# Performance work log

Measured on AMD Instinct MI355X. Metric: run time of the kernel, lower is better.

## Reference

```python
import jax, jax.numpy as jnp
import numpy as np

B, T, D, G, E, V = 32, 1024, 512, 256, 8, 8192


def setup_inputs() -> dict:
    key = jax.random.key(0)
    k1, k2, k3, k4, k5 = jax.random.split(key, 5)
    return {
        "gate_features": jax.random.normal(k1, (B, G), dtype=jnp.float32),
        "input_features": jax.random.normal(k2, (B, T, D), dtype=jnp.float32),
        "Wg": jax.random.normal(k3, (G, E), dtype=jnp.float32) * 0.02,
        "bg": jnp.zeros((E,), dtype=jnp.float32),
        "We": jax.random.normal(k4, (E, D, V), dtype=jnp.float32) * 0.02,
        "be": jnp.zeros((E, V), dtype=jnp.float32),
        "target_ids": jax.random.randint(k5, (B, T), 0, V, dtype=jnp.int64),
    }


def reference(gate_features, input_features, Wg, bg, We, be, target_ids):
    # ---- Router: linear gate -> softmax probs -> top-1 assignment ----
    router_logits = gate_features @ Wg + bg            # [B, E]
    probs = jax.nn.softmax(router_logits, axis=-1)     # [B, E]
    assignments = jnp.argmax(router_logits, axis=-1)   # [B]

    # ---- Dispatch: gather each sample's expert parameters ----
    W_sel = We[assignments]                            # [B, D, V]
    b_sel = be[assignments]                            # [B, V]

    # ---- Expert compute: linear LM head + cross-entropy loss ----
    logits = jnp.einsum("btd,bdv->btv", input_features, W_sel) + b_sel[:, None, :]
    logp = jax.nn.log_softmax(logits, axis=-1)         # [B, T, V]
    nll = -jnp.take_along_axis(logp, target_ids[..., None], axis=-1)[..., 0]  # [B, T]
    ce_per_sample = nll.mean(axis=-1)                  # [B]

    # ---- Combine: total_loss = sum over experts of per-expert mean loss ----
    sums = jax.ops.segment_sum(ce_per_sample, assignments, num_segments=E)   # [E]
    counts = jax.ops.segment_sum(jnp.ones_like(ce_per_sample), assignments, num_segments=E)
    loss_per_expert = jnp.where(counts > 0, sums / jnp.maximum(counts, 1.0), 0.0)
    total_loss = loss_per_expert.sum()

    return total_loss, assignments, probs
```

## Files before the change

kernel.cpp:

```cpp
#include <hip/hip_runtime.h>

#define NB 32
#define NT 1024
#define ND 512
#define NG 256
#define NE 8
#define NV 8192
#define NROW (NB * NT)

#define XBF_BYTES   (33554432)
#define WT_BYTES    (67108864)
#define PSUM_BYTES  (8388608)
#define TL_BYTES    (131072)

#define BM2 256
#define BN2 256
#define NCT (NV / BN2)

typedef float f32x4 __attribute__((ext_vector_type(4)));
typedef __bf16 bf16x8 __attribute__((ext_vector_type(8)));
typedef unsigned short ushort8_v __attribute__((ext_vector_type(8)));
typedef unsigned int u32_g __attribute__((address_space(1)));
typedef unsigned int u32_l __attribute__((address_space(3)));
typedef unsigned short ushort_t;

__device__ __forceinline__ void g2l16(void* lds, const void* g) {
    __builtin_amdgcn_global_load_lds((const u32_g*)g, (u32_l*)lds, 16, 0, 0);
}

__device__ __forceinline__ unsigned short f2bf(float f) {
    unsigned int u = __float_as_uint(f);
    unsigned int r = (u + 0x7fffu + ((u >> 16) & 1u)) >> 16;
    return (unsigned short)r;
}

__global__ void k_convx(const float4* __restrict__ in, ushort_t* __restrict__ out4, int n4,
                        const float* __restrict__ gate, const float* __restrict__ Wg,
                        const float* __restrict__ bg, float* __restrict__ out,
                        int* __restrict__ assign, int* __restrict__ counts) {
    int tid = threadIdx.x;
    if (blockIdx.x == 0) {
        __shared__ float lg[NB][NE];
        __shared__ int lam[NB];
        int b = tid >> 3, e = tid & 7;
        float acc = bg[e];
        const float* gr = gate + b * NG;
        for (int g = 0; g < NG; ++g) acc = fmaf(gr[g], Wg[g * NE + e], acc);
        lg[b][e] = acc;
        __syncthreads();
        if (tid < NB) {
            float mx = lg[tid][0]; int am = 0;
            for (int j = 1; j < NE; ++j) { float v = lg[tid][j]; if (v > mx) { mx = v; am = j; } }
            float den = 0.f, ex[NE];
            for (int j = 0; j < NE; ++j) { ex[j] = __expf(lg[tid][j] - mx); den += ex[j]; }
            float inv = 1.f / den;
            for (int j = 0; j < NE; ++j) out[1 + NB + tid * NE + j] = ex[j] * inv;
            out[1 + tid] = (float)am;
            assign[tid] = am;
            lam[tid] = am;
        }
        __syncthreads();
        if (tid == 0) {
            int c[NE] = {0,0,0,0,0,0,0,0};
            for (int i = 0; i < NB; ++i) c[lam[i]]++;
            for (int j = 0; j < NE; ++j) counts[j] = c[j];
            out[0] = 0.f;
        }
    }
    int i = blockIdx.x * blockDim.x + tid;
    int stride = gridDim.x * blockDim.x;
    for (; i < n4; i += stride) {
        float4 v = in[i];
        ushort4 o;
        o.x = f2bf(v.x); o.y = f2bf(v.y); o.z = f2bf(v.z); o.w = f2bf(v.w);
        ((ushort4*)out4)[i] = o;
    }
}

__global__ void k_transw(const float* __restrict__ We, ushort_t* __restrict__ Wt) {
    __shared__ float tile[64][68];
    int e = blockIdx.z, d0 = blockIdx.y * 64, v0 = blockIdx.x * 64;
    int tid = threadIdx.x;
    const float* src = We + (size_t)e * ND * NV + (size_t)d0 * NV + v0;
    int dr = tid >> 4;
    int c4 = tid & 15;
#pragma unroll
    for (int j = 0; j < 4; ++j) {
        int d = dr + 16 * j;
        float4 v = *(const float4*)(src + (size_t)d * NV + c4 * 4);
        *(float4*)&tile[d][((c4 ^ (d >> 3)) & 15) * 4] = v;
    }
    __syncthreads();
    ushort_t* dst = Wt + (size_t)e * NV * ND + (size_t)v0 * ND + d0;
    int vr = tid >> 3;
    int t8 = tid & 7;
#pragma unroll
    for (int j = 0; j < 2; ++j) {
        int v = vr + 32 * j;
        ushort8_v o;
#pragma unroll
        for (int i = 0; i < 8; ++i)
            o[i] = f2bf(tile[t8 * 8 + i][(((v >> 2) ^ t8) & 15) * 4 + (v & 3)]);
        *(ushort8_v*)(dst + (size_t)v * ND + t8 * 8) = o;
    }
}


#define BAR_MID() do { \
    asm volatile("" ::: "memory"); \
    __builtin_amdgcn_s_barrier(); \
    asm volatile("s_waitcnt lgkmcnt(0)" ::: "memory"); \
    __builtin_amdgcn_sched_barrier(0); } while (0)

#define BAR_END() do { \
    asm volatile("" ::: "memory"); \
    __builtin_amdgcn_s_barrier(); \
    asm volatile("" ::: "memory"); } while (0)

#define MFMA_QUAD(MH, NH) do { \
    __builtin_amdgcn_s_setprio(1); \
    _Pragma("unroll") \
    for (int m_ = 0; m_ < 4; ++m_) \
      _Pragma("unroll") \
      for (int n_ = 0; n_ < 2; ++n_) \
        _Pragma("unroll") \
        for (int ks_ = 0; ks_ < 2; ++ks_) \
          acc[(MH) * 4 + m_][(NH) * 2 + n_] = __builtin_amdgcn_mfma_f32_16x16x32_bf16( \
              af[m_][ks_], bfr[(NH) * 2 + n_][ks_], acc[(MH) * 4 + m_][(NH) * 2 + n_], 0, 0, 0); \
    __builtin_amdgcn_s_setprio(0); } while (0)

__global__ __launch_bounds__(512, 2)
void k_gemm(const ushort_t* __restrict__ Xbf, const ushort_t* __restrict__ Wtbf,
            const float* __restrict__ be, const int* __restrict__ assign,
            const int* __restrict__ tgt, float* __restrict__ psum,
            float* __restrict__ tl) {
    __shared__ alignas(16) char smem[136192];
    float* lws = (float*)(smem + 131072);
    int*   lt  = (int*)(smem + 135168);

    const int tid  = threadIdx.x;
    const int wid  = tid >> 6, lane = tid & 63;
    const int q = lane >> 4, ln = lane & 15;
    const int wr = wid >> 2, wc = wid & 3;

    const int bid = blockIdx.x;
    const int wg  = ((bid & 7) << 9) | (bid >> 3);
    const int ct  = wg >> 7;
    const int rt  = wg & 127;
    const int e   = assign[rt >> 2];
    const size_t eV = (size_t)e * NV;

    const int rquo = tid >> 3;
    const int scol = ((tid & 7) ^ (rquo & 7)) << 3;
    const ushort_t* gA = Xbf + (size_t)(rt * BM2 + rquo) * ND + scol;
    const ushort_t* gB = Wtbf + (eV + ct * BN2 + rquo) * ND + scol;
    char* ldsW = smem + wid * 1024;
    const int axor = ln & 7;

    if (tid < 256) lt[tid] = tgt[rt * BM2 + tid];

    f32x4 acc[8][4];
#pragma unroll
    for (int i = 0; i < 8; ++i)
#pragma unroll
        for (int j = 0; j < 4; ++j) acc[i][j] = (f32x4){0.f, 0.f, 0.f, 0.f};

#define STA(KT, BP, H) do { \
    char* d_ = ldsW + (BP) * 65536 + (H) * 16384; \
    const ushort_t* g_ = gA + (size_t)(H) * 128 * ND + (KT) * 64; \
    g2l16(d_, g_); g2l16(d_ + 8192, g_ + (size_t)64 * ND); } while (0)

#define STB(KT, BP, H) do { \
    char* d_ = ldsW + (BP) * 65536 + 32768 + (H) * 16384; \
    const ushort_t* g_ = gB + (size_t)(H) * 128 * ND + (KT) * 64; \
    g2l16(d_, g_); g2l16(d_ + 8192, g_ + (size_t)64 * ND); } while (0)

#define RDA(BP, MF, KS) \
    (*(const bf16x8*)(smem + (BP) * 65536 + wr * 16384 + \
                      ((MF) * 16 + ln) * 128 + ((((KS) * 4 + q) ^ axor) << 4)))

#define RDB(BP, NF, KS) \
    (*(const bf16x8*)(smem + (BP) * 65536 + 32768 + (wc >> 1) * 16384 + \
                      (((wc & 1) * 64 + (NF) * 16 + ln) * 128) + ((((KS) * 4 + q) ^ axor) << 4)))

    STB(0, 0, 0); STB(0, 0, 1); STA(0, 0, 0); STA(0, 0, 1);
    STB(1, 1, 0); STB(1, 1, 1);
    asm volatile("s_waitcnt vmcnt(4)" ::: "memory");
    __builtin_amdgcn_s_barrier();
    asm volatile("" ::: "memory");

    bf16x8 af[4][2];
    bf16x8 bfr[4][2];

#pragma unroll
    for (int kt = 0; kt < 8; ++kt) {
        const int p = kt & 1, np = p ^ 1;

#pragma unroll
        for (int m = 0; m < 4; ++m) { af[m][0] = RDA(p, m, 0); af[m][1] = RDA(p, m, 1); }
#pragma unroll
        for (int n = 0; n < 2; ++n) { bfr[n][0] = RDB(p, n, 0); bfr[n][1] = RDB(p, n, 1); }
        if (kt < 7) STA(kt + 1, np, 0);
        BAR_MID();
        MFMA_QUAD(0, 0);
        BAR_END();

#pragma unroll
        for (int n = 0; n < 2; ++n) { bfr[2 + n][0] = RDB(p, 2 + n, 0); bfr[2 + n][1] = RDB(p, 2 + n, 1); }
        if (kt < 7) STA(kt + 1, np, 1);
        BAR_MID();
        MFMA_QUAD(0, 1);
        BAR_END();

#pragma unroll
        for (int m = 0; m < 4; ++m) { af[m][0] = RDA(p, 4 + m, 0); af[m][1] = RDA(p, 4 + m, 1); }
        if (kt < 6) STB(kt + 2, p, 0);
        BAR_MID();
        MFMA_QUAD(1, 1);
        BAR_END();

        if (kt < 6) STB(kt + 2, p, 1);
        BAR_MID();
        MFMA_QUAD(1, 0);
        if (kt < 6)       { asm volatile("s_waitcnt vmcnt(4)" ::: "memory"); }
        else if (kt == 6) { asm volatile("s_waitcnt vmcnt(0)" ::: "memory"); }
        BAR_END();
    }

    const float LOG2E = 1.44269504088896f;
    int tcv[8][4];
#pragma unroll
    for (int mf = 0; mf < 8; ++mf)
#pragma unroll
        for (int r = 0; r < 4; ++r)
            tcv[mf][r] = lt[wr * 128 + mf * 16 + q * 4 + r];

    float partial[32];
#pragma unroll
    for (int i = 0; i < 32; ++i) partial[i] = 0.f;
#pragma unroll
    for (int nf = 0; nf < 4; ++nf) {
        int col = (ct << 8) + (wc << 6) + nf * 16 + ln;
        float br = be[eV + col];
        float eb = br * LOG2E;
#pragma unroll
        for (int mf = 0; mf < 8; ++mf)
#pragma unroll
            for (int r = 0; r < 4; ++r) {
                partial[mf * 4 + r] += exp2f(fmaf(acc[mf][nf][r], LOG2E, eb));
                if (col == tcv[mf][r])
                    tl[rt * BM2 + wr * 128 + mf * 16 + q * 4 + r] = acc[mf][nf][r] + br;
            }
    }
#pragma unroll
    for (int i = 0; i < 32; ++i) {
        float pv = partial[i];
        pv += __shfl_xor(pv, 1); pv += __shfl_xor(pv, 2);
        pv += __shfl_xor(pv, 4); pv += __shfl_xor(pv, 8);
        partial[i] = pv;
    }
    if (ln == 0) {
#pragma unroll
        for (int mf = 0; mf < 8; ++mf)
#pragma unroll
            for (int r = 0; r < 4; ++r)
                lws[wid * 128 + mf * 16 + q * 4 + r] = partial[mf * 4 + r];
    }
    __syncthreads();
    if (tid < 256) {
        int wrh = tid >> 7, idx = tid & 127;
        float s = lws[(wrh * 4 + 0) * 128 + idx] + lws[(wrh * 4 + 1) * 128 + idx]
                + lws[(wrh * 4 + 2) * 128 + idx] + lws[(wrh * 4 + 3) * 128 + idx];
        psum[(size_t)ct * NROW + rt * 256 + tid] = s;
    }
#undef STA
#undef STB
#undef RDA
#undef RDB
}

__global__ void k_loss(const float* __restrict__ psum, const float* __restrict__ tl,
                       const int* __restrict__ assign, const int* __restrict__ counts,
                       float* __restrict__ out) {
    int b = blockIdx.x, tid = threadIdx.x;
    float acc = 0.f;
#pragma unroll
    for (int j = 0; j < 4; ++j) {
        int t = j * 256 + tid;
        float s = 0.f;
        for (int ct = 0; ct < NCT; ++ct) s += psum[(size_t)ct * NROW + b * NT + t];
        acc += __logf(s) - tl[b * NT + t];
    }
    __shared__ float red[4];
    for (int off = 32; off; off >>= 1) acc += __shfl_down(acc, off);
    if ((tid & 63) == 0) red[tid >> 6] = acc;
    __syncthreads();
    if (tid == 0) {
        float nb = red[0] + red[1] + red[2] + red[3];
        float ce = nb * (1.0f / (float)NT);
        atomicAdd(out, ce / (float)counts[assign[b]]);
    }
}

extern "C" void kernel_launch(void* const* d_in, const int* in_sizes, int n_in,
                              void* d_out, int out_size, void* d_ws, size_t ws_size,
                              hipStream_t stream) {
    const float* gate = (const float*)d_in[0];
    const float* X    = (const float*)d_in[1];
    const float* Wg   = (const float*)d_in[2];
    const float* bg   = (const float*)d_in[3];
    const float* We   = (const float*)d_in[4];
    const float* be   = (const float*)d_in[5];
    const int*   tgt  = (const int*)d_in[6];
    float* out = (float*)d_out;

    char* ws = (char*)d_ws;
    ushort_t* Xbf  = (ushort_t*)ws;
    ushort_t* Wtbf = (ushort_t*)(ws + XBF_BYTES);
    float*    psum = (float*)(ws + XBF_BYTES + WT_BYTES);
    float*    tl   = (float*)(ws + XBF_BYTES + WT_BYTES + PSUM_BYTES);
    int*      assign = (int*)(ws + XBF_BYTES + WT_BYTES + PSUM_BYTES + TL_BYTES);
    int*      counts = assign + 32;

    k_convx<<<4096, 256, 0, stream>>>((const float4*)X, Xbf, NB * NT * ND / 4,
                                      gate, Wg, bg, out, assign, counts);
    k_transw<<<dim3(NV / 64, ND / 64, NE), 256, 0, stream>>>(We, Wtbf);
    k_gemm<<<(NROW / BM2) * (NV / BN2), 512, 0, stream>>>(Xbf, Wtbf, be, assign, tgt, psum, tl);
    k_loss<<<NB, 256, 0, stream>>>(psum, tl, assign, counts, out);
}
```

Baseline: 608.4 us.

## Merge weight transpose and input conversion into one prep kernel, stage bias/targets via LDS

```diff
diff --git a/kernel.cpp b/kernel.cpp
--- a/kernel.cpp
+++ b/kernel.cpp
@@ -34,74 +34,77 @@
     return (unsigned short)r;
 }
 
-__global__ void k_convx(const float4* __restrict__ in, ushort_t* __restrict__ out4, int n4,
-                        const float* __restrict__ gate, const float* __restrict__ Wg,
-                        const float* __restrict__ bg, float* __restrict__ out,
-                        int* __restrict__ assign, int* __restrict__ counts) {
-    int tid = threadIdx.x;
-    if (blockIdx.x == 0) {
-        __shared__ float lg[NB][NE];
-        __shared__ int lam[NB];
-        int b = tid >> 3, e = tid & 7;
-        float acc = bg[e];
-        const float* gr = gate + b * NG;
-        for (int g = 0; g < NG; ++g) acc = fmaf(gr[g], Wg[g * NE + e], acc);
-        lg[b][e] = acc;
-        __syncthreads();
-        if (tid < NB) {
-            float mx = lg[tid][0]; int am = 0;
-            for (int j = 1; j < NE; ++j) { float v = lg[tid][j]; if (v > mx) { mx = v; am = j; } }
-            float den = 0.f, ex[NE];
-            for (int j = 0; j < NE; ++j) { ex[j] = __expf(lg[tid][j] - mx); den += ex[j]; }
-            float inv = 1.f / den;
-            for (int j = 0; j < NE; ++j) out[1 + NB + tid * NE + j] = ex[j] * inv;
-            out[1 + tid] = (float)am;
-            assign[tid] = am;
-            lam[tid] = am;
+__global__ __launch_bounds__(256)
+void k_prep(const float* __restrict__ We, ushort_t* __restrict__ Wt,
+            const float4* __restrict__ X, ushort_t* __restrict__ Xbf, int n4,
+            const float* __restrict__ gate, const float* __restrict__ Wg,
+            const float* __restrict__ bg, float* __restrict__ out,
+            int* __restrict__ assign, int* __restrict__ counts) {
+    int bid = blockIdx.x, tid = threadIdx.x;
+    if (bid < 8192) {
+        __shared__ float tile[64][68];
+        int e = bid >> 10, rem = bid & 1023;
+        int d0 = (rem >> 7) << 6;
+        int v0 = (rem & 127) << 6;
+        const float* src = We + (size_t)e * ND * NV + (size_t)d0 * NV + v0;
+        int dr = tid >> 4;
+        int c4 = tid & 15;
+#pragma unroll
+        for (int j = 0; j < 4; ++j) {
+            int d = dr + 16 * j;
+            float4 v = *(const float4*)(src + (size_t)d * NV + c4 * 4);
+            *(float4*)&tile[d][((c4 ^ (d >> 3)) & 15) * 4] = v;
         }
         __syncthreads();
-        if (tid == 0) {
-            int c[NE] = {0,0,0,0,0,0,0,0};
-            for (int i = 0; i < NB; ++i) c[lam[i]]++;
-            for (int j = 0; j < NE; ++j) counts[j] = c[j];
-            out[0] = 0.f;
+        ushort_t* dst = Wt + (size_t)e * NV * ND + (size_t)v0 * ND + d0;
+        int vr = tid >> 3;
+        int t8 = tid & 7;
+#pragma unroll
+        for (int j = 0; j < 2; ++j) {
+            int v = vr + 32 * j;
+            ushort8_v o;
+#pragma unroll
+            for (int i = 0; i < 8; ++i)
+                o[i] = f2bf(tile[t8 * 8 + i][(((v >> 2) ^ t8) & 15) * 4 + (v & 3)]);
+            *(ushort8_v*)(dst + (size_t)v * ND + t8 * 8) = o;
         }
-    }
-    int i = blockIdx.x * blockDim.x + tid;
-    int stride = gridDim.x * blockDim.x;
-    for (; i < n4; i += stride) {
-        float4 v = in[i];
-        ushort4 o;
-        o.x = f2bf(v.x); o.y = f2bf(v.y); o.z = f2bf(v.z); o.w = f2bf(v.w);
-        ((ushort4*)out4)[i] = o;
-    }
-}
-
-__global__ void k_transw(const float* __restrict__ We, ushort_t* __restrict__ Wt) {
-    __shared__ float tile[64][68];
-    int e = blockIdx.z, d0 = blockIdx.y * 64, v0 = blockIdx.x * 64;
-    int tid = threadIdx.x;
-    const float* src = We + (size_t)e * ND * NV + (size_t)d0 * NV + v0;
-    int dr = tid >> 4;
-    int c4 = tid & 15;
-#pragma unroll
-    for (int j = 0; j < 4; ++j) {
-        int d = dr + 16 * j;
-        float4 v = *(const float4*)(src + (size_t)d * NV + c4 * 4);
-        *(float4*)&tile[d][((c4 ^ (d >> 3)) & 15) * 4] = v;
-    }
-    __syncthreads();
-    ushort_t* dst = Wt + (size_t)e * NV * ND + (size_t)v0 * ND + d0;
-    int vr = tid >> 3;
-    int t8 = tid & 7;
-#pragma unroll
-    for (int j = 0; j < 2; ++j) {
-        int v = vr + 32 * j;
-        ushort8_v o;
-#pragma unroll
-        for (int i = 0; i < 8; ++i)
-            o[i] = f2bf(tile[t8 * 8 + i][(((v >> 2) ^ t8) & 15) * 4 + (v & 3)]);
-        *(ushort8_v*)(dst + (size_t)v * ND + t8 * 8) = o;
+    } else {
+        if (bid == 8192) {
+            __shared__ float lg[NB][NE];
+            __shared__ int lam[NB];
+            int b = tid >> 3, e = tid & 7;
+            float acc = bg[e];
+            const float* gr = gate + b * NG;
+            for (int g = 0; g < NG; ++g) acc = fmaf(gr[g], Wg[g * NE + e], acc);
+            lg[b][e] = acc;
+            __syncthreads();
+            if (tid < NB) {
+                float mx = lg[tid][0]; int am = 0;
+                for (int j = 1; j < NE; ++j) { float v = lg[tid][j]; if (v > mx) { mx = v; am = j; } }
+                float den = 0.f, ex[NE];
+                for (int j = 0; j < NE; ++j) { ex[j] = __expf(lg[tid][j] - mx); den += ex[j]; }
+                float inv = 1.f / den;
+                for (int j = 0; j < NE; ++j) out[1 + NB + tid * NE + j] = ex[j] * inv;
+                out[1 + tid] = (float)am;
+                assign[tid] = am;
+                lam[tid] = am;
+            }
+            __syncthreads();
+            if (tid == 0) {
+                int c[NE] = {0,0,0,0,0,0,0,0};
+                for (int i = 0; i < NB; ++i) c[lam[i]]++;
+                for (int j = 0; j < NE; ++j) counts[j] = c[j];
+                out[0] = 0.f;
+            }
+        }
+        int i = (bid - 8192) * 256 + tid;
+        int stride = 4096 * 256;
+        for (; i < n4; i += stride) {
+            float4 v = X[i];
+            ushort4 o;
+            o.x = f2bf(v.x); o.y = f2bf(v.y); o.z = f2bf(v.z); o.w = f2bf(v.w);
+            ((ushort4*)Xbf)[i] = o;
+        }
     }
 }
 
@@ -134,9 +137,10 @@
             const float* __restrict__ be, const int* __restrict__ assign,
             const int* __restrict__ tgt, float* __restrict__ psum,
             float* __restrict__ tl) {
-    __shared__ alignas(16) char smem[136192];
+    __shared__ alignas(16) char smem[137216];
     float* lws = (float*)(smem + 131072);
-    int*   lt  = (int*)(smem + 135168);
+    float* lbe = (float*)(smem + 135168);
+    int*   lt  = (int*)(smem + 136192);
 
     const int tid  = threadIdx.x;
     const int wid  = tid >> 6, lane = tid & 63;
@@ -157,8 +161,6 @@
     char* ldsW = smem + wid * 1024;
     const int axor = ln & 7;
 
-    if (tid < 256) lt[tid] = tgt[rt * BM2 + tid];
-
     f32x4 acc[8][4];
 #pragma unroll
     for (int i = 0; i < 8; ++i)
@@ -182,6 +184,9 @@
 #define RDB(BP, NF, KS) \
     (*(const bf16x8*)(smem + (BP) * 65536 + 32768 + (wc >> 1) * 16384 + \
                       (((wc & 1) * 64 + (NF) * 16 + ln) * 128) + ((((KS) * 4 + q) ^ axor) << 4)))
+
+    if (wid == 0) g2l16(smem + 135168, be + eV + (ct << 8) + (lane << 2));
+    if (wid == 1) g2l16(smem + 136192, tgt + rt * BM2 + (lane << 2));
 
     STB(0, 0, 0); STB(0, 0, 1); STA(0, 0, 0); STA(0, 0, 1);
     STB(1, 1, 0); STB(1, 1, 1);
@@ -228,30 +233,41 @@
     }
 
     const float LOG2E = 1.44269504088896f;
-    int tcv[8][4];
-#pragma unroll
-    for (int mf = 0; mf < 8; ++mf)
-#pragma unroll
-        for (int r = 0; r < 4; ++r)
-            tcv[mf][r] = lt[wr * 128 + mf * 16 + q * 4 + r];
+    float lbev[4];
+#pragma unroll
+    for (int nf = 0; nf < 4; ++nf) lbev[nf] = lbe[(wc << 6) + nf * 16 + ln];
 
     float partial[32];
 #pragma unroll
     for (int i = 0; i < 32; ++i) partial[i] = 0.f;
 #pragma unroll
     for (int nf = 0; nf < 4; ++nf) {
-        int col = (ct << 8) + (wc << 6) + nf * 16 + ln;
-        float br = be[eV + col];
-        float eb = br * LOG2E;
+        float eb = lbev[nf] * LOG2E;
 #pragma unroll
         for (int mf = 0; mf < 8; ++mf)
 #pragma unroll
+            for (int r = 0; r < 4; ++r)
+                partial[mf * 4 + r] += exp2f(fmaf(acc[mf][nf][r], LOG2E, eb));
+    }
+
+    {
+        const int cb = (ct << 8) + (wc << 6);
+#pragma unroll
+        for (int mf = 0; mf < 8; ++mf)
+#pragma unroll
             for (int r = 0; r < 4; ++r) {
-                partial[mf * 4 + r] += exp2f(fmaf(acc[mf][nf][r], LOG2E, eb));
-                if (col == tcv[mf][r])
-                    tl[rt * BM2 + wr * 128 + mf * 16 + q * 4 + r] = acc[mf][nf][r] + br;
+                int local = lt[wr * 128 + mf * 16 + q * 4 + r] - cb;
+                if ((unsigned)local < 64u && (local & 15) == ln) {
+                    int nfi = local >> 4;
+                    float v = (nfi == 0) ? acc[mf][0][r]
+                            : (nfi == 1) ? acc[mf][1][r]
+                            : (nfi == 2) ? acc[mf][2][r]
+                            :              acc[mf][3][r];
+                    tl[rt * BM2 + wr * 128 + mf * 16 + q * 4 + r] = v + lbe[(wc << 6) + local];
+                }
             }
     }
+
 #pragma unroll
     for (int i = 0; i < 32; ++i) {
         float pv = partial[i];
@@ -322,9 +338,8 @@
     int*      assign = (int*)(ws + XBF_BYTES + WT_BYTES + PSUM_BYTES + TL_BYTES);
     int*      counts = assign + 32;
 
-    k_convx<<<4096, 256, 0, stream>>>((const float4*)X, Xbf, NB * NT * ND / 4,
+    k_prep<<<12288, 256, 0, stream>>>(We, Wtbf, (const float4*)X, Xbf, NB * NT * ND / 4,
                                       gate, Wg, bg, out, assign, counts);
-    k_transw<<<dim3(NV / 64, ND / 64, NE), 256, 0, stream>>>(We, Wtbf);
     k_gemm<<<(NROW / BM2) * (NV / BN2), 512, 0, stream>>>(Xbf, Wtbf, be, assign, tgt, psum, tl);
     k_loss<<<NB, 256, 0, stream>>>(psum, tl, assign, counts, out);
 }
```

Measured after the change: 577.2 us. 5.1% less time.
